# Performance work log

Measured on AMD Instinct MI355X. Metric: run time of the kernel, lower is better.

Reference implementation:

```python
import jax, jax.numpy as jnp
import numpy as np

CDECAY = 0.5      # NEURON_CDECAY = 1/2
VDECAY = 0.75     # NEURON_VDECAY = 3/4
VTH_INIT = 0.5
T = 50            # batch_window
sg = jax.lax.stop_gradient


@jax.custom_vjp
def pseudo_spike(v, vth):
    return (v > vth).astype(v.dtype)

def _ps_fwd(v, vth):
    return pseudo_spike(v, vth), (v, vth)

def _ps_bwd(res, g):
    v, vth = res
    # PseudoSpikeRect: rectangular surrogate gradient, window 0.5; no grad to vth
    return (g * (jnp.abs(v - vth) < 0.5).astype(g.dtype), jnp.zeros_like(vth))

pseudo_spike.defvjp(_ps_fwd, _ps_bwd)


def lif_step(x_in, W, b, u, v_prev, s_prev, temporal):
    """One neuron_model_* call + the temporal-threshold update that follows it."""
    u = u * CDECAY + x_in @ W.T + b
    v = v_prev * VDECAY * (1.0 - s_prev) + u
    # energy threshold term uses detached volts in the original (numpy round-trip)
    energy = jnp.exp((sg(v_prev) - sg(v)) / 3.0) - 1.0
    vth = 0.5 * temporal + 0.5 * energy
    s = pseudo_spike(v, vth)
    vsg = sg(v)  # threshold chain never reaches the loss (custom fn has no vth grad)
    V_m = vsg.mean() - 0.2 * (vsg.max() - vsg.min())
    V_theta = vth.mean() - 0.2 * (vth.max() - vth.min())
    temporal_new = 0.01 * (vsg - V_m) + V_theta + jnp.log(1.0 + jnp.exp((vsg - V_m) / 4.0))
    return u, v, s, temporal_new


def _forward(x, fc1_u, fc1_v, fc1_s, fc2_u, fc2_v, fc2_s, fc3_u, fc3_v, fc3_s,
             fc4_u, fc4_v, fc4_s, W1, b1, W2, b2, W3, b3, W4, b4):
    B = x.shape[0]
    H = W1.shape[0]
    A = W4.shape[0]
    t1 = jnp.full((B, H), VTH_INIT, x.dtype)
    t2 = jnp.full((B, H), VTH_INIT, x.dtype)
    t3 = jnp.full((B, H), VTH_INIT, x.dtype)
    t4 = jnp.full((B, A), VTH_INIT, x.dtype)
    acc = jnp.zeros((B, A), x.dtype)
    xs = jnp.transpose(x, (2, 0, 1))  # [T, B, state_num]

    def step(carry, xt):
        (u1, v1, s1, tt1, u2, v2, s2, tt2, u3, v3, s3, tt3, u4, v4, s4, tt4, a) = carry
        u1, v1, s1, tt1 = lif_step(xt, W1, b1, u1, v1, s1, tt1)
        u2, v2, s2, tt2 = lif_step(s1, W2, b2, u2, v2, s2, tt2)
        u3, v3, s3, tt3 = lif_step(s2, W3, b3, u3, v3, s3, tt3)
        u4, v4, s4, tt4 = lif_step(s3, W4, b4, u4, v4, s4, tt4)
        a = a + s4
        return (u1, v1, s1, tt1, u2, v2, s2, tt2, u3, v3, s3, tt3, u4, v4, s4, tt4, a), None

    carry0 = (fc1_u, fc1_v, fc1_s, t1, fc2_u, fc2_v, fc2_s, t2,
              fc3_u, fc3_v, fc3_s, t3, fc4_u, fc4_v, fc4_s, t4, acc)
    carry, _ = jax.lax.scan(step, carry0, xs)
    return carry[-1] / T  # fc4_sumspike / batch_window


def setup_inputs() -> dict:
    key = jax.random.key(0)
    ks = jax.random.split(key, 10)
    B, S, H, A = 2048, 256, 256, 2
    inp = {"x": jax.random.normal(ks[0], (B, S, T), jnp.float32)}
    for name, shp in [("fc1_u", (B, H)), ("fc1_v", (B, H)), ("fc1_s", (B, H)),
                      ("fc2_u", (B, H)), ("fc2_v", (B, H)), ("fc2_s", (B, H)),
                      ("fc3_u", (B, H)), ("fc3_v", (B, H)), ("fc3_s", (B, H)),
                      ("fc4_u", (B, A)), ("fc4_v", (B, A)), ("fc4_s", (B, A))]:
        inp[name] = jnp.zeros(shp, jnp.float32)
    def lin(k, fan_out, fan_in):
        bound = 1.0 / np.sqrt(fan_in)
        kw, kb = jax.random.split(k)
        W = jax.random.uniform(kw, (fan_out, fan_in), jnp.float32, -bound, bound)
        b = jax.random.uniform(kb, (fan_out,), jnp.float32, -bound, bound)
        return W, b
    inp["W1"], inp["b1"] = lin(ks[1], H, S)
    inp["W2"], inp["b2"] = lin(ks[2], H, H)
    inp["W3"], inp["b3"] = lin(ks[3], H, H)
    inp["W4"], inp["b4"] = lin(ks[4], A, H)
    inp["batch_size"] = B
    return inp


def reference(x, fc1_u, fc1_v, fc1_s, fc2_u, fc2_v, fc2_s, fc3_u, fc3_v, fc3_s,
              fc4_u, fc4_v, fc4_s, W1, b1, W2, b2, W3, b3, W4, b4, batch_size):
    return _forward(x, fc1_u, fc1_v, fc1_s, fc2_u, fc2_v, fc2_s,
                    fc3_u, fc3_v, fc3_s, fc4_u, fc4_v, fc4_s,
                    W1, b1, W2, b2, W3, b3, W4, b4)
```

## Files before the change

kernel.cpp:

```cpp
#include <hip/hip_runtime.h>
#include <cstdint>
#include <cstddef>

#define BB 2048
#define SS 256
#define HH 256
#define AA 2
#define TT 50
#define ROWS  32
#define NTHR  512
#define NLG   64
#define NGRID 192
#define KSTR  272
#define WLAYER (256 * KSTR)
#define LSTR  36
#define S3P   260

struct Params {
  const float* x;
  const float* fu[3]; const float* fv[3]; const float* fs[3];
  const float* f4u; const float* f4v; const float* f4s;
  const float* W[3]; const float* bs[3];
  const float* W4; const float* b4;
  float* out;
  float* wt3;
  float* partials;
  unsigned* flags;
  float* sbuf;
  float* xT;
  int use_xt;
};

__device__ __forceinline__ void pstore(float* p, float v) {
  __hip_atomic_store(p, v, __ATOMIC_RELAXED, __HIP_MEMORY_SCOPE_AGENT);
}
__device__ __forceinline__ float pload(const float* p) {
  return __hip_atomic_load(p, __ATOMIC_RELAXED, __HIP_MEMORY_SCOPE_AGENT);
}
__device__ __forceinline__ unsigned uload_acq(const unsigned* p) {
  return __hip_atomic_load(p, __ATOMIC_ACQUIRE, __HIP_MEMORY_SCOPE_AGENT);
}
__device__ __forceinline__ void ustore_rel(unsigned* p, unsigned v) {
  __hip_atomic_store(p, v, __ATOMIC_RELEASE, __HIP_MEMORY_SCOPE_AGENT);
}
__device__ __forceinline__ void uadd(unsigned* p) {
  __hip_atomic_fetch_add(p, 1u, __ATOMIC_ACQ_REL, __HIP_MEMORY_SCOPE_AGENT);
}

#define OUTER(IV, WV)                                        \
  acc[0][0] = fmaf((IV).x, (WV).x, acc[0][0]);               \
  acc[0][1] = fmaf((IV).x, (WV).y, acc[0][1]);               \
  acc[0][2] = fmaf((IV).x, (WV).z, acc[0][2]);               \
  acc[0][3] = fmaf((IV).x, (WV).w, acc[0][3]);               \
  acc[1][0] = fmaf((IV).y, (WV).x, acc[1][0]);               \
  acc[1][1] = fmaf((IV).y, (WV).y, acc[1][1]);               \
  acc[1][2] = fmaf((IV).y, (WV).z, acc[1][2]);               \
  acc[1][3] = fmaf((IV).y, (WV).w, acc[1][3]);               \
  acc[2][0] = fmaf((IV).z, (WV).x, acc[2][0]);               \
  acc[2][1] = fmaf((IV).z, (WV).y, acc[2][1]);               \
  acc[2][2] = fmaf((IV).z, (WV).z, acc[2][2]);               \
  acc[2][3] = fmaf((IV).z, (WV).w, acc[2][3]);               \
  acc[3][0] = fmaf((IV).w, (WV).x, acc[3][0]);               \
  acc[3][1] = fmaf((IV).w, (WV).y, acc[3][1]);               \
  acc[3][2] = fmaf((IV).w, (WV).z, acc[3][2]);               \
  acc[3][3] = fmaf((IV).w, (WV).w, acc[3][3]);

__global__ __launch_bounds__(NTHR, 2)
void snn_pipe(Params p) {
#pragma clang fp contract(off)
  const int tid = threadIdx.x;
  const int blk = blockIdx.x;
  const int L   = blk >> 6;
  const int g   = blk & 63;
  const int B0  = g * ROWS;

  const int w    = tid >> 6;
  const int l    = tid & 63;
  const int hp   = w & 3;
  const int qp   = w >> 2;
  const int hsel = l & 15;
  const int jsel = l >> 4;
  const int hb   = hp * 64 + hsel * 4;
  const int jb   = qp * 16 + jsel * 4;

  const int sid = tid & 255;
  const int jq  = tid >> 8;

  __shared__ __align__(16) float in_lds[HH * LSTR];
  __shared__ __align__(16) float s3_lds[ROWS * S3P];
  __shared__ float wred[8][6];
  __shared__ float scal[2][2];
  __shared__ float l4u[64], l4v[64], l4s[64], l4t[64],
                   l4acc[64], l4vn[64], l4vth[64];

  {
    const int gtid = blk * NTHR + tid;
    if (gtid < 16384) {
      const int h = gtid & 255, kq = gtid >> 8;
      #pragma unroll
      for (int ll = 0; ll < 3; ++ll) {
        float4 wv = *reinterpret_cast<const float4*>(p.W[ll] + (size_t)h * 256 + kq * 4);
        float* dst = p.wt3 + (size_t)ll * WLAYER + (size_t)(kq * 4) * KSTR + h;
        dst[0 * KSTR] = wv.x; dst[1 * KSTR] = wv.y;
        dst[2 * KSTR] = wv.z; dst[3 * KSTR] = wv.w;
      }
    }
    if (p.use_xt) {
      for (int sid0 = gtid; sid0 < BB * SS; sid0 += NGRID * NTHR) {
        const float* src = p.x + (size_t)sid0 * TT;
        #pragma unroll 1
        for (int t = 0; t < TT; ++t)
          p.xT[(size_t)t * (BB * SS) + sid0] = src[t];
      }
    }
  }

  float u[4][4], v[4][4], tp[4][4];
  unsigned smask = 0;
  #pragma unroll
  for (int jj = 0; jj < 4; ++jj) {
    size_t idx = (size_t)(B0 + jb + jj) * HH + hb;
    float4 uu = *reinterpret_cast<const float4*>(p.fu[L] + idx);
    float4 vv = *reinterpret_cast<const float4*>(p.fv[L] + idx);
    float4 ss = *reinterpret_cast<const float4*>(p.fs[L] + idx);
    u[jj][0] = uu.x; u[jj][1] = uu.y; u[jj][2] = uu.z; u[jj][3] = uu.w;
    v[jj][0] = vv.x; v[jj][1] = vv.y; v[jj][2] = vv.z; v[jj][3] = vv.w;
    if (ss.x != 0.0f) smask |= 1u << (jj * 4 + 0);
    if (ss.y != 0.0f) smask |= 1u << (jj * 4 + 1);
    if (ss.z != 0.0f) smask |= 1u << (jj * 4 + 2);
    if (ss.w != 0.0f) smask |= 1u << (jj * 4 + 3);
    #pragma unroll
    for (int i = 0; i < 4; ++i) tp[jj][i] = 0.5f;
  }
  const float4 bb4 = *reinterpret_cast<const float4*>(p.bs[L] + hb);
  const float bL[4] = { bb4.x, bb4.y, bb4.z, bb4.w };
  if (L == 2 && tid < 64) {
    size_t idx = (size_t)(B0 + (tid >> 1)) * AA + (tid & 1);
    l4u[tid] = p.f4u[idx]; l4v[tid] = p.f4v[idx]; l4s[tid] = p.f4s[idx];
    l4t[tid] = 0.5f; l4acc[tid] = 0.0f;
  }
  __syncthreads();

  if (tid == 0) {
    uadd(&p.flags[260]);
    while (uload_acq(&p.flags[260]) < (unsigned)NGRID) __builtin_amdgcn_s_sleep(2);
  }
  __syncthreads();

  const float* wbase = p.wt3 + (size_t)L * WLAYER + hb;
  float* sb_in  = (L > 0) ? p.sbuf + (size_t)(L - 1) * 2 * BB * HH : nullptr;
  float* sb_out = (L < 2) ? p.sbuf + (size_t)L * 2 * BB * HH : nullptr;

  #pragma unroll 1
  for (int t = 0; t < TT; ++t) {
    if (L == 0) {
      if (p.use_xt) {
        const float* base = p.xT + (size_t)t * (BB * SS) + (size_t)B0 * SS;
        #pragma unroll
        for (int iq = 0; iq < 4; ++iq) {
          const int j = jq * 16 + iq * 4;
          float4 vv = make_float4(base[(size_t)(j + 0) * SS + sid],
                                  base[(size_t)(j + 1) * SS + sid],
                                  base[(size_t)(j + 2) * SS + sid],
                                  base[(size_t)(j + 3) * SS + sid]);
          *reinterpret_cast<float4*>(&in_lds[sid * LSTR + j]) = vv;
        }
      } else {
        #pragma unroll
        for (int iq = 0; iq < 4; ++iq) {
          const int j = jq * 16 + iq * 4;
          float4 vv = make_float4(
              p.x[((size_t)(B0 + j + 0) * SS + sid) * TT + t],
              p.x[((size_t)(B0 + j + 1) * SS + sid) * TT + t],
              p.x[((size_t)(B0 + j + 2) * SS + sid) * TT + t],
              p.x[((size_t)(B0 + j + 3) * SS + sid) * TT + t]);
          *reinterpret_cast<float4*>(&in_lds[sid * LSTR + j]) = vv;
        }
      }
    } else {
      const int hop = L - 1;
      if (tid == 0) {
        while (uload_acq(&p.flags[hop * 64 + g]) < (unsigned)(t + 1))
          __builtin_amdgcn_s_sleep(2);
      }
      __syncthreads();
      const float* src = sb_in + (size_t)(t & 1) * BB * HH;
      #pragma unroll
      for (int iq = 0; iq < 4; ++iq) {
        const int j = jq * 16 + iq * 4;
        float4 vv = make_float4(pload(src + (size_t)(B0 + j + 0) * HH + sid),
                                pload(src + (size_t)(B0 + j + 1) * HH + sid),
                                pload(src + (size_t)(B0 + j + 2) * HH + sid),
                                pload(src + (size_t)(B0 + j + 3) * HH + sid));
        *reinterpret_cast<float4*>(&in_lds[sid * LSTR + j]) = vv;
      }
      __syncthreads();
      if (tid == 0) ustore_rel(&p.flags[128 + hop * 64 + g], (unsigned)(t + 1));
    }
    __syncthreads();

    float acc[4][4];
    #pragma unroll
    for (int jj = 0; jj < 4; ++jj)
      #pragma unroll
      for (int i = 0; i < 4; ++i) acc[jj][i] = 0.0f;
    #pragma unroll 2
    for (int k4 = 0; k4 < 64; ++k4) {
      const float* wk = wbase + (size_t)(k4 * 4) * KSTR;
      float4 w0 = *reinterpret_cast<const float4*>(wk);
      float4 w1 = *reinterpret_cast<const float4*>(wk + KSTR);
      float4 w2 = *reinterpret_cast<const float4*>(wk + 2 * KSTR);
      float4 w3 = *reinterpret_cast<const float4*>(wk + 3 * KSTR);
      const float* ib = &in_lds[(k4 * 4) * LSTR + jb];
      float4 i0 = *reinterpret_cast<const float4*>(ib);
      float4 i1 = *reinterpret_cast<const float4*>(ib + LSTR);
      float4 i2 = *reinterpret_cast<const float4*>(ib + 2 * LSTR);
      float4 i3 = *reinterpret_cast<const float4*>(ib + 3 * LSTR);
      OUTER(i0, w0);
      OUTER(i1, w1);
      OUTER(i2, w2);
      OUTER(i3, w3);
    }

    if (t > 0) {
      if (tid == 0) {
        while (uload_acq(&p.flags[256 + L]) < (unsigned)(NLG * t))
          __builtin_amdgcn_s_sleep(2);
      }
      __syncthreads();
      {
        const int wv = tid >> 6, ln = tid & 63;
        if (wv == 0 || (wv == 1 && L == 2)) {
          const int ch = (wv == 0) ? L : 3;
          const float* pb = p.partials + (size_t)(ch * 2 + ((t - 1) & 1)) * 6 * 64;
          float r[6];
          #pragma unroll
          for (int st = 0; st < 6; ++st) {
            float rr = pload(pb + st * 64 + ln);
            if (st == 0 || st == 3) {
              #pragma unroll
              for (int m = 1; m < 64; m <<= 1) rr += __shfl_xor(rr, m);
            } else if (st == 1 || st == 4) {
              #pragma unroll
              for (int m = 1; m < 64; m <<= 1) rr = fmaxf(rr, __shfl_xor(rr, m));
            } else {
              #pragma unroll
              for (int m = 1; m < 64; m <<= 1) rr = fminf(rr, __shfl_xor(rr, m));
            }
            r[st] = rr;
          }
          if (ln == 0) {
            const float invN = (ch == 3) ? (1.0f / 4096.0f) : (1.0f / 524288.0f);
            scal[wv][0] = (r[0] * invN) - 0.2f * (r[1] - r[2]);
            scal[wv][1] = (r[3] * invN) - 0.2f * (r[4] - r[5]);
          }
        }
      }
      __syncthreads();
      {
        const float Vm = scal[0][0], Vt = scal[0][1];
        #pragma unroll
        for (int jj = 0; jj < 4; ++jj)
          #pragma unroll
          for (int i = 0; i < 4; ++i) {
            float d = v[jj][i] - Vm;
            float sp = logf(1.0f + expf(d * 0.25f));
            tp[jj][i] = (0.01f * d + Vt) + sp;
          }
      }
      if (L == 2 && tid < 64) {
        const float Vm = scal[1][0], Vt = scal[1][1];
        float d = l4v[tid] - Vm;
        float sp = logf(1.0f + expf(d * 0.25f));
        l4t[tid] = (0.01f * d + Vt) + sp;
      }
      __syncthreads();
    }

    float sv = 0.f, svt = 0.f;
    float mxv = -3.402823466e38f, mnv = 3.402823466e38f;
    float mxvt = -3.402823466e38f, mnvt = 3.402823466e38f;
    unsigned nsmask = 0;
    #pragma unroll
    for (int jj = 0; jj < 4; ++jj) {
      #pragma unroll
      for (int i = 0; i < 4; ++i) {
        float un = fmaf(u[jj][i], 0.5f, acc[jj][i]) + bL[i];
        float vp = v[jj][i];
        float vd = ((smask >> (jj * 4 + i)) & 1u) ? 0.0f : vp * 0.75f;
        float vn = vd + un;
        float en = expf((vp - vn) / 3.0f) - 1.0f;
        float vt = 0.5f * tp[jj][i] + 0.5f * en;
        const bool sx = vn > vt;
        u[jj][i] = un; v[jj][i] = vn;
        if (sx) nsmask |= 1u << (jj * 4 + i);
        sv += vn; svt += vt;
        mxv = fmaxf(mxv, vn); mnv = fminf(mnv, vn);
        mxvt = fmaxf(mxvt, vt); mnvt = fminf(mnvt, vt);
      }
    }
    smask = nsmask;
    #pragma unroll
    for (int m = 1; m < 64; m <<= 1) {
      sv += __shfl_xor(sv, m);   svt += __shfl_xor(svt, m);
      mxv = fmaxf(mxv, __shfl_xor(mxv, m));  mnv = fminf(mnv, __shfl_xor(mnv, m));
      mxvt = fmaxf(mxvt, __shfl_xor(mxvt, m)); mnvt = fminf(mnvt, __shfl_xor(mnvt, m));
    }
    if ((tid & 63) == 0) {
      int wv = tid >> 6;
      wred[wv][0] = sv;  wred[wv][1] = mxv;  wred[wv][2] = mnv;
      wred[wv][3] = svt; wred[wv][4] = mxvt; wred[wv][5] = mnvt;
    }
    #pragma unroll
    for (int jj = 0; jj < 4; ++jj) {
      *reinterpret_cast<float4*>(&s3_lds[(jb + jj) * S3P + hb]) = make_float4(
          ((nsmask >> (jj * 4 + 0)) & 1u) ? 1.0f : 0.0f,
          ((nsmask >> (jj * 4 + 1)) & 1u) ? 1.0f : 0.0f,
          ((nsmask >> (jj * 4 + 2)) & 1u) ? 1.0f : 0.0f,
          ((nsmask >> (jj * 4 + 3)) & 1u) ? 1.0f : 0.0f);
    }
    __syncthreads();

    if (L < 2) {
      if (tid < 6) {
        const int st = tid;
        float r = wred[0][st];
        if (st == 0 || st == 3) {
          #pragma unroll
          for (int wv = 1; wv < 8; ++wv) r = r + wred[wv][st];
        } else if (st == 1 || st == 4) {
          #pragma unroll
          for (int wv = 1; wv < 8; ++wv) r = fmaxf(r, wred[wv][st]);
        } else {
          #pragma unroll
          for (int wv = 1; wv < 8; ++wv) r = fminf(r, wred[wv][st]);
        }
        pstore(p.partials + (size_t)(L * 2 + (t & 1)) * 6 * 64 + st * 64 + g, r);
      }
      if (t >= 2 && tid == 1) {
        while (uload_acq(&p.flags[128 + L * 64 + g]) < (unsigned)(t - 1))
          __builtin_amdgcn_s_sleep(2);
      }
      __syncthreads();
      if (tid == 0) uadd(&p.flags[256 + L]);
      float* dst = sb_out + (size_t)(t & 1) * BB * HH;
      #pragma unroll
      for (int jr = 0; jr < 16; ++jr) {
        const int j = jq * 16 + jr;
        pstore(dst + (size_t)(B0 + j) * HH + sid, s3_lds[j * S3P + sid]);
      }
      __syncthreads();
      if (tid == 0) ustore_rel(&p.flags[L * 64 + g], (unsigned)(t + 1));
    } else {
      if (tid < 6) {
        const int st = tid;
        float r = wred[0][st];
        if (st == 0 || st == 3) {
          #pragma unroll
          for (int wv = 1; wv < 8; ++wv) r = r + wred[wv][st];
        } else if (st == 1 || st == 4) {
          #pragma unroll
          for (int wv = 1; wv < 8; ++wv) r = fmaxf(r, wred[wv][st]);
        } else {
          #pragma unroll
          for (int wv = 1; wv < 8; ++wv) r = fminf(r, wred[wv][st]);
        }
        pstore(p.partials + (size_t)(2 * 2 + (t & 1)) * 6 * 64 + st * 64 + g, r);
      }
      __syncthreads();

      {
        const int d = tid >> 3, c = tid & 7;
        if (d < 64) {
          const int j4 = d >> 1, a4 = d & 1;
          float part = 0.0f;
          #pragma unroll
          for (int i = 0; i < 32; ++i) {
            int k = c + 8 * i;
            part = fmaf(s3_lds[j4 * S3P + k], p.W4[a4 * HH + k], part);
          }
          #pragma unroll
          for (int m = 1; m < 8; m <<= 1) part += __shfl_xor(part, m);
          if (c == 0) {
            float un = fmaf(l4u[d], 0.5f, part) + p.b4[a4];
            float vp = l4v[d];
            float vd = (vp * 0.75f) * (1.0f - l4s[d]);
            float vn = vd + un;
            float en = expf((vp - vn) / 3.0f) - 1.0f;
            float vt = 0.5f * l4t[d] + 0.5f * en;
            float sx = (vn > vt) ? 1.0f : 0.0f;
            l4u[d] = un; l4v[d] = vn; l4s[d] = sx;
            l4acc[d] += sx; l4vn[d] = vn; l4vth[d] = vt;
          }
        }
      }
      __syncthreads();

      if (tid < 64) {
        float a = l4vn[tid], b = l4vth[tid];
        float s4 = a, mx4 = a, mn4 = a;
        float st4 = b, mxt4 = b, mnt4 = b;
        #pragma unroll
        for (int m = 1; m < 64; m <<= 1) {
          s4  += __shfl_xor(s4, m);   st4 += __shfl_xor(st4, m);
          mx4  = fmaxf(mx4,  __shfl_xor(mx4, m));  mn4  = fminf(mn4,  __shfl_xor(mn4, m));
          mxt4 = fmaxf(mxt4, __shfl_xor(mxt4, m)); mnt4 = fminf(mnt4, __shfl_xor(mnt4, m));
        }
        if (tid == 0) {
          float* pp = p.partials + (size_t)(3 * 2 + (t & 1)) * 6 * 64 + g;
          pstore(pp + 0 * 64, s4);   pstore(pp + 1 * 64, mx4);  pstore(pp + 2 * 64, mn4);
          pstore(pp + 3 * 64, st4);  pstore(pp + 4 * 64, mxt4); pstore(pp + 5 * 64, mnt4);
        }
      }
      __syncthreads();
      if (tid == 0) uadd(&p.flags[256 + L]);
    }
  }

  if (L == 2 && tid < 64)
    p.out[(size_t)(B0 + (tid >> 1)) * AA + (tid & 1)] = l4acc[tid] / 50.0f;
}

extern "C" void kernel_launch(void* const* d_in, const int* in_sizes, int n_in,
                              void* d_out, int out_size, void* d_ws, size_t ws_size,
                              hipStream_t stream) {
  Params p;
  p.x     = (const float*)d_in[0];
  p.fu[0] = (const float*)d_in[1];  p.fv[0] = (const float*)d_in[2];  p.fs[0] = (const float*)d_in[3];
  p.fu[1] = (const float*)d_in[4];  p.fv[1] = (const float*)d_in[5];  p.fs[1] = (const float*)d_in[6];
  p.fu[2] = (const float*)d_in[7];  p.fv[2] = (const float*)d_in[8];  p.fs[2] = (const float*)d_in[9];
  p.f4u   = (const float*)d_in[10]; p.f4v   = (const float*)d_in[11]; p.f4s   = (const float*)d_in[12];
  p.W[0]  = (const float*)d_in[13]; p.bs[0] = (const float*)d_in[14];
  p.W[1]  = (const float*)d_in[15]; p.bs[1] = (const float*)d_in[16];
  p.W[2]  = (const float*)d_in[17]; p.bs[2] = (const float*)d_in[18];
  p.W4    = (const float*)d_in[19]; p.b4    = (const float*)d_in[20];
  p.out   = (float*)d_out;

  float* ws   = (float*)d_ws;
  p.wt3       = ws;
  p.partials  = ws + 208896;
  p.flags     = (unsigned*)(ws + 211968);
  p.sbuf      = ws + 212992;
  p.xT        = ws + 2310144;
  size_t need = ((size_t)2310144 + (size_t)TT * BB * SS) * sizeof(float);
  p.use_xt    = (ws_size >= need) ? 1 : 0;

  hipMemsetAsync((void*)p.flags, 0, 4096, stream);
  snn_pipe<<<dim3(NGRID), dim3(NTHR), 0, stream>>>(p);
}
```

Measured before the change: 1.890 ms.

## Split layer 4 into its own pipeline stage and pass spikes as bytes

Adds a fourth group of 64 blocks, raising the grid from 192 to 256, so the small output layer (fc4) runs as its own pipeline stage instead of being serialized behind layer 3 inside the same blocks. Inter-stage spike buffers switch from float to uint8, cutting the handoff traffic through global memory by a factor of four, and the flag and workspace layout are re-indexed to match. The extra stage adds another hop of synchronisation latency and needs all 256 blocks to be co-resident for the spin-wait barriers to avoid deadlock.

```diff
diff --git a/kernel.cpp b/kernel.cpp
--- a/kernel.cpp
+++ b/kernel.cpp
@@ -10,7 +10,7 @@
 #define ROWS  32
 #define NTHR  512
 #define NLG   64
-#define NGRID 192
+#define NGRID 256
 #define KSTR  272
 #define WLAYER (256 * KSTR)
 #define LSTR  36
@@ -26,7 +26,7 @@
   float* wt3;
   float* partials;
   unsigned* flags;
-  float* sbuf;
+  uint8_t* sbuf;
   float* xT;
   int use_xt;
 };
@@ -35,6 +35,12 @@
   __hip_atomic_store(p, v, __ATOMIC_RELAXED, __HIP_MEMORY_SCOPE_AGENT);
 }
 __device__ __forceinline__ float pload(const float* p) {
+  return __hip_atomic_load(p, __ATOMIC_RELAXED, __HIP_MEMORY_SCOPE_AGENT);
+}
+__device__ __forceinline__ void bstore(uint8_t* p, uint8_t v) {
+  __hip_atomic_store(p, v, __ATOMIC_RELAXED, __HIP_MEMORY_SCOPE_AGENT);
+}
+__device__ __forceinline__ uint8_t bload(const uint8_t* p) {
   return __hip_atomic_load(p, __ATOMIC_RELAXED, __HIP_MEMORY_SCOPE_AGENT);
 }
 __device__ __forceinline__ unsigned uload_acq(const unsigned* p) {
@@ -73,6 +79,7 @@
   const int L   = blk >> 6;
   const int g   = blk & 63;
   const int B0  = g * ROWS;
+  const int LW  = (L < 3) ? L : 2;
 
   const int w    = tid >> 6;
   const int l    = tid & 63;
@@ -89,7 +96,7 @@
   __shared__ __align__(16) float in_lds[HH * LSTR];
   __shared__ __align__(16) float s3_lds[ROWS * S3P];
   __shared__ float wred[8][6];
-  __shared__ float scal[2][2];
+  __shared__ float scal[2];
   __shared__ float l4u[64], l4v[64], l4s[64], l4t[64],
                    l4acc[64], l4vn[64], l4vth[64];
 
@@ -116,25 +123,27 @@
   }
 
   float u[4][4], v[4][4], tp[4][4];
+  float bL[4] = {0.f, 0.f, 0.f, 0.f};
   unsigned smask = 0;
-  #pragma unroll
-  for (int jj = 0; jj < 4; ++jj) {
-    size_t idx = (size_t)(B0 + jb + jj) * HH + hb;
-    float4 uu = *reinterpret_cast<const float4*>(p.fu[L] + idx);
-    float4 vv = *reinterpret_cast<const float4*>(p.fv[L] + idx);
-    float4 ss = *reinterpret_cast<const float4*>(p.fs[L] + idx);
-    u[jj][0] = uu.x; u[jj][1] = uu.y; u[jj][2] = uu.z; u[jj][3] = uu.w;
-    v[jj][0] = vv.x; v[jj][1] = vv.y; v[jj][2] = vv.z; v[jj][3] = vv.w;
-    if (ss.x != 0.0f) smask |= 1u << (jj * 4 + 0);
-    if (ss.y != 0.0f) smask |= 1u << (jj * 4 + 1);
-    if (ss.z != 0.0f) smask |= 1u << (jj * 4 + 2);
-    if (ss.w != 0.0f) smask |= 1u << (jj * 4 + 3);
+  if (L < 3) {
     #pragma unroll
-    for (int i = 0; i < 4; ++i) tp[jj][i] = 0.5f;
-  }
-  const float4 bb4 = *reinterpret_cast<const float4*>(p.bs[L] + hb);
-  const float bL[4] = { bb4.x, bb4.y, bb4.z, bb4.w };
-  if (L == 2 && tid < 64) {
+    for (int jj = 0; jj < 4; ++jj) {
+      size_t idx = (size_t)(B0 + jb + jj) * HH + hb;
+      float4 uu = *reinterpret_cast<const float4*>(p.fu[LW] + idx);
+      float4 vv = *reinterpret_cast<const float4*>(p.fv[LW] + idx);
+      float4 ss = *reinterpret_cast<const float4*>(p.fs[LW] + idx);
+      u[jj][0] = uu.x; u[jj][1] = uu.y; u[jj][2] = uu.z; u[jj][3] = uu.w;
+      v[jj][0] = vv.x; v[jj][1] = vv.y; v[jj][2] = vv.z; v[jj][3] = vv.w;
+      if (ss.x != 0.0f) smask |= 1u << (jj * 4 + 0);
+      if (ss.y != 0.0f) smask |= 1u << (jj * 4 + 1);
+      if (ss.z != 0.0f) smask |= 1u << (jj * 4 + 2);
+      if (ss.w != 0.0f) smask |= 1u << (jj * 4 + 3);
+      #pragma unroll
+      for (int i = 0; i < 4; ++i) tp[jj][i] = 0.5f;
+    }
+    float4 bb4 = *reinterpret_cast<const float4*>(p.bs[LW] + hb);
+    bL[0] = bb4.x; bL[1] = bb4.y; bL[2] = bb4.z; bL[3] = bb4.w;
+  } else if (tid < 64) {
     size_t idx = (size_t)(B0 + (tid >> 1)) * AA + (tid & 1);
     l4u[tid] = p.f4u[idx]; l4v[tid] = p.f4v[idx]; l4s[tid] = p.f4s[idx];
     l4t[tid] = 0.5f; l4acc[tid] = 0.0f;
@@ -142,101 +151,102 @@
   __syncthreads();
 
   if (tid == 0) {
-    uadd(&p.flags[260]);
-    while (uload_acq(&p.flags[260]) < (unsigned)NGRID) __builtin_amdgcn_s_sleep(2);
+    uadd(&p.flags[520]);
+    while (uload_acq(&p.flags[520]) < (unsigned)NGRID) __builtin_amdgcn_s_sleep(2);
   }
   __syncthreads();
 
-  const float* wbase = p.wt3 + (size_t)L * WLAYER + hb;
-  float* sb_in  = (L > 0) ? p.sbuf + (size_t)(L - 1) * 2 * BB * HH : nullptr;
-  float* sb_out = (L < 2) ? p.sbuf + (size_t)L * 2 * BB * HH : nullptr;
+  const float* wbase = p.wt3 + (size_t)LW * WLAYER + hb;
+  const uint8_t* sb_in = (L > 0) ? p.sbuf + (size_t)(L - 1) * 2 * BB * HH : nullptr;
+  uint8_t* sb_out      = (L < 3) ? p.sbuf + (size_t)L * 2 * BB * HH : nullptr;
 
   #pragma unroll 1
   for (int t = 0; t < TT; ++t) {
-    if (L == 0) {
-      if (p.use_xt) {
-        const float* base = p.xT + (size_t)t * (BB * SS) + (size_t)B0 * SS;
-        #pragma unroll
-        for (int iq = 0; iq < 4; ++iq) {
-          const int j = jq * 16 + iq * 4;
-          float4 vv = make_float4(base[(size_t)(j + 0) * SS + sid],
-                                  base[(size_t)(j + 1) * SS + sid],
-                                  base[(size_t)(j + 2) * SS + sid],
-                                  base[(size_t)(j + 3) * SS + sid]);
-          *reinterpret_cast<float4*>(&in_lds[sid * LSTR + j]) = vv;
+    const int par = t & 1;
+
+    if (L < 3) {
+      if (L == 0) {
+        if (p.use_xt) {
+          const float* base = p.xT + (size_t)t * (BB * SS) + (size_t)B0 * SS;
+          #pragma unroll
+          for (int iq = 0; iq < 4; ++iq) {
+            const int j = jq * 16 + iq * 4;
+            float4 vv = make_float4(base[(size_t)(j + 0) * SS + sid],
+                                    base[(size_t)(j + 1) * SS + sid],
+                                    base[(size_t)(j + 2) * SS + sid],
+                                    base[(size_t)(j + 3) * SS + sid]);
+            *reinterpret_cast<float4*>(&in_lds[sid * LSTR + j]) = vv;
+          }
+        } else {
+          #pragma unroll
+          for (int iq = 0; iq < 4; ++iq) {
+            const int j = jq * 16 + iq * 4;
+            float4 vv = make_float4(
+                p.x[((size_t)(B0 + j + 0) * SS + sid) * TT + t],
+                p.x[((size_t)(B0 + j + 1) * SS + sid) * TT + t],
+                p.x[((size_t)(B0 + j + 2) * SS + sid) * TT + t],
+                p.x[((size_t)(B0 + j + 3) * SS + sid) * TT + t]);
+            *reinterpret_cast<float4*>(&in_lds[sid * LSTR + j]) = vv;
+          }
         }
       } else {
+        const int hop = L - 1;
+        if (tid == 0) {
+          while (uload_acq(&p.flags[hop * 64 + g]) < (unsigned)(t + 1))
+            __builtin_amdgcn_s_sleep(2);
+        }
+        __syncthreads();
+        const uint8_t* src = sb_in + (size_t)par * BB * HH;
         #pragma unroll
         for (int iq = 0; iq < 4; ++iq) {
           const int j = jq * 16 + iq * 4;
           float4 vv = make_float4(
-              p.x[((size_t)(B0 + j + 0) * SS + sid) * TT + t],
-              p.x[((size_t)(B0 + j + 1) * SS + sid) * TT + t],
-              p.x[((size_t)(B0 + j + 2) * SS + sid) * TT + t],
-              p.x[((size_t)(B0 + j + 3) * SS + sid) * TT + t]);
+              (float)bload(src + (size_t)(B0 + j + 0) * HH + sid),
+              (float)bload(src + (size_t)(B0 + j + 1) * HH + sid),
+              (float)bload(src + (size_t)(B0 + j + 2) * HH + sid),
+              (float)bload(src + (size_t)(B0 + j + 3) * HH + sid));
           *reinterpret_cast<float4*>(&in_lds[sid * LSTR + j]) = vv;
         }
-      }
-    } else {
-      const int hop = L - 1;
-      if (tid == 0) {
-        while (uload_acq(&p.flags[hop * 64 + g]) < (unsigned)(t + 1))
-          __builtin_amdgcn_s_sleep(2);
-      }
-      __syncthreads();
-      const float* src = sb_in + (size_t)(t & 1) * BB * HH;
-      #pragma unroll
-      for (int iq = 0; iq < 4; ++iq) {
-        const int j = jq * 16 + iq * 4;
-        float4 vv = make_float4(pload(src + (size_t)(B0 + j + 0) * HH + sid),
-                                pload(src + (size_t)(B0 + j + 1) * HH + sid),
-                                pload(src + (size_t)(B0 + j + 2) * HH + sid),
-                                pload(src + (size_t)(B0 + j + 3) * HH + sid));
-        *reinterpret_cast<float4*>(&in_lds[sid * LSTR + j]) = vv;
-      }
-      __syncthreads();
-      if (tid == 0) ustore_rel(&p.flags[128 + hop * 64 + g], (unsigned)(t + 1));
-    }
-    __syncthreads();
-
-    float acc[4][4];
-    #pragma unroll
-    for (int jj = 0; jj < 4; ++jj)
-      #pragma unroll
-      for (int i = 0; i < 4; ++i) acc[jj][i] = 0.0f;
-    #pragma unroll 2
-    for (int k4 = 0; k4 < 64; ++k4) {
-      const float* wk = wbase + (size_t)(k4 * 4) * KSTR;
-      float4 w0 = *reinterpret_cast<const float4*>(wk);
-      float4 w1 = *reinterpret_cast<const float4*>(wk + KSTR);
-      float4 w2 = *reinterpret_cast<const float4*>(wk + 2 * KSTR);
-      float4 w3 = *reinterpret_cast<const float4*>(wk + 3 * KSTR);
-      const float* ib = &in_lds[(k4 * 4) * LSTR + jb];
-      float4 i0 = *reinterpret_cast<const float4*>(ib);
-      float4 i1 = *reinterpret_cast<const float4*>(ib + LSTR);
-      float4 i2 = *reinterpret_cast<const float4*>(ib + 2 * LSTR);
-      float4 i3 = *reinterpret_cast<const float4*>(ib + 3 * LSTR);
-      OUTER(i0, w0);
-      OUTER(i1, w1);
-      OUTER(i2, w2);
-      OUTER(i3, w3);
-    }
-
-    if (t > 0) {
-      if (tid == 0) {
-        while (uload_acq(&p.flags[256 + L]) < (unsigned)(NLG * t))
-          __builtin_amdgcn_s_sleep(2);
-      }
-      __syncthreads();
-      {
-        const int wv = tid >> 6, ln = tid & 63;
-        if (wv == 0 || (wv == 1 && L == 2)) {
-          const int ch = (wv == 0) ? L : 3;
-          const float* pb = p.partials + (size_t)(ch * 2 + ((t - 1) & 1)) * 6 * 64;
+        __syncthreads();
+        if (tid == 0) ustore_rel(&p.flags[256 + hop * 64 + g], (unsigned)(t + 1));
+      }
+      __syncthreads();
+
+      float acc[4][4];
+      #pragma unroll
+      for (int jj = 0; jj < 4; ++jj)
+        #pragma unroll
+        for (int i = 0; i < 4; ++i) acc[jj][i] = 0.0f;
+      #pragma unroll 2
+      for (int k4 = 0; k4 < 64; ++k4) {
+        const float* wk = wbase + (size_t)(k4 * 4) * KSTR;
+        float4 w0 = *reinterpret_cast<const float4*>(wk);
+        float4 w1 = *reinterpret_cast<const float4*>(wk + KSTR);
+        float4 w2 = *reinterpret_cast<const float4*>(wk + 2 * KSTR);
+        float4 w3 = *reinterpret_cast<const float4*>(wk + 3 * KSTR);
+        const float* ib = &in_lds[(k4 * 4) * LSTR + jb];
+        float4 i0 = *reinterpret_cast<const float4*>(ib);
+        float4 i1 = *reinterpret_cast<const float4*>(ib + LSTR);
+        float4 i2 = *reinterpret_cast<const float4*>(ib + 2 * LSTR);
+        float4 i3 = *reinterpret_cast<const float4*>(ib + 3 * LSTR);
+        OUTER(i0, w0);
+        OUTER(i1, w1);
+        OUTER(i2, w2);
+        OUTER(i3, w3);
+      }
+
+      if (t > 0) {
+        if (tid == 0) {
+          while (uload_acq(&p.flags[512 + L]) < (unsigned)(NLG * t))
+            __builtin_amdgcn_s_sleep(2);
+        }
+        __syncthreads();
+        if (w == 0) {
+          const float* pb = p.partials + (size_t)(L * 2 + ((t - 1) & 1)) * 6 * 64;
           float r[6];
           #pragma unroll
           for (int st = 0; st < 6; ++st) {
-            float rr = pload(pb + st * 64 + ln);
+            float rr = pload(pb + st * 64 + l);
             if (st == 0 || st == 3) {
               #pragma unroll
               for (int m = 1; m < 64; m <<= 1) rr += __shfl_xor(rr, m);
@@ -249,16 +259,14 @@
             }
             r[st] = rr;
           }
-          if (ln == 0) {
-            const float invN = (ch == 3) ? (1.0f / 4096.0f) : (1.0f / 524288.0f);
-            scal[wv][0] = (r[0] * invN) - 0.2f * (r[1] - r[2]);
-            scal[wv][1] = (r[3] * invN) - 0.2f * (r[4] - r[5]);
-          }
-        }
-      }
-      __syncthreads();
-      {
-        const float Vm = scal[0][0], Vt = scal[0][1];
+          if (l == 0) {
+            const float invN = 1.0f / 524288.0f;
+            scal[0] = (r[0] * invN) - 0.2f * (r[1] - r[2]);
+            scal[1] = (r[3] * invN) - 0.2f * (r[4] - r[5]);
+          }
+        }
+        __syncthreads();
+        const float Vm = scal[0], Vt = scal[1];
         #pragma unroll
         for (int jj = 0; jj < 4; ++jj)
           #pragma unroll
@@ -267,61 +275,53 @@
             float sp = logf(1.0f + expf(d * 0.25f));
             tp[jj][i] = (0.01f * d + Vt) + sp;
           }
-      }
-      if (L == 2 && tid < 64) {
-        const float Vm = scal[1][0], Vt = scal[1][1];
-        float d = l4v[tid] - Vm;
-        float sp = logf(1.0f + expf(d * 0.25f));
-        l4t[tid] = (0.01f * d + Vt) + sp;
-      }
-      __syncthreads();
-    }
-
-    float sv = 0.f, svt = 0.f;
-    float mxv = -3.402823466e38f, mnv = 3.402823466e38f;
-    float mxvt = -3.402823466e38f, mnvt = 3.402823466e38f;
-    unsigned nsmask = 0;
-    #pragma unroll
-    for (int jj = 0; jj < 4; ++jj) {
-      #pragma unroll
-      for (int i = 0; i < 4; ++i) {
-        float un = fmaf(u[jj][i], 0.5f, acc[jj][i]) + bL[i];
-        float vp = v[jj][i];
-        float vd = ((smask >> (jj * 4 + i)) & 1u) ? 0.0f : vp * 0.75f;
-        float vn = vd + un;
-        float en = expf((vp - vn) / 3.0f) - 1.0f;
-        float vt = 0.5f * tp[jj][i] + 0.5f * en;
-        const bool sx = vn > vt;
-        u[jj][i] = un; v[jj][i] = vn;
-        if (sx) nsmask |= 1u << (jj * 4 + i);
-        sv += vn; svt += vt;
-        mxv = fmaxf(mxv, vn); mnv = fminf(mnv, vn);
-        mxvt = fmaxf(mxvt, vt); mnvt = fminf(mnvt, vt);
-      }
-    }
-    smask = nsmask;
-    #pragma unroll
-    for (int m = 1; m < 64; m <<= 1) {
-      sv += __shfl_xor(sv, m);   svt += __shfl_xor(svt, m);
-      mxv = fmaxf(mxv, __shfl_xor(mxv, m));  mnv = fminf(mnv, __shfl_xor(mnv, m));
-      mxvt = fmaxf(mxvt, __shfl_xor(mxvt, m)); mnvt = fminf(mnvt, __shfl_xor(mnvt, m));
-    }
-    if ((tid & 63) == 0) {
-      int wv = tid >> 6;
-      wred[wv][0] = sv;  wred[wv][1] = mxv;  wred[wv][2] = mnv;
-      wred[wv][3] = svt; wred[wv][4] = mxvt; wred[wv][5] = mnvt;
-    }
-    #pragma unroll
-    for (int jj = 0; jj < 4; ++jj) {
-      *reinterpret_cast<float4*>(&s3_lds[(jb + jj) * S3P + hb]) = make_float4(
-          ((nsmask >> (jj * 4 + 0)) & 1u) ? 1.0f : 0.0f,
-          ((nsmask >> (jj * 4 + 1)) & 1u) ? 1.0f : 0.0f,
-          ((nsmask >> (jj * 4 + 2)) & 1u) ? 1.0f : 0.0f,
-          ((nsmask >> (jj * 4 + 3)) & 1u) ? 1.0f : 0.0f);
-    }
-    __syncthreads();
-
-    if (L < 2) {
+        __syncthreads();
+      }
+
+      float sv = 0.f, svt = 0.f;
+      float mxv = -3.402823466e38f, mnv = 3.402823466e38f;
+      float mxvt = -3.402823466e38f, mnvt = 3.402823466e38f;
+      unsigned nsmask = 0;
+      #pragma unroll
+      for (int jj = 0; jj < 4; ++jj) {
+        #pragma unroll
+        for (int i = 0; i < 4; ++i) {
+          float un = fmaf(u[jj][i], 0.5f, acc[jj][i]) + bL[i];
+          float vp = v[jj][i];
+          float vd = ((smask >> (jj * 4 + i)) & 1u) ? 0.0f : vp * 0.75f;
+          float vn = vd + un;
+          float en = expf((vp - vn) / 3.0f) - 1.0f;
+          float vt = 0.5f * tp[jj][i] + 0.5f * en;
+          const bool sx = vn > vt;
+          u[jj][i] = un; v[jj][i] = vn;
+          if (sx) nsmask |= 1u << (jj * 4 + i);
+          sv += vn; svt += vt;
+          mxv = fmaxf(mxv, vn); mnv = fminf(mnv, vn);
+          mxvt = fmaxf(mxvt, vt); mnvt = fminf(mnvt, vt);
+        }
+      }
+      smask = nsmask;
+      #pragma unroll
+      for (int m = 1; m < 64; m <<= 1) {
+        sv += __shfl_xor(sv, m);   svt += __shfl_xor(svt, m);
+        mxv = fmaxf(mxv, __shfl_xor(mxv, m));  mnv = fminf(mnv, __shfl_xor(mnv, m));
+        mxvt = fmaxf(mxvt, __shfl_xor(mxvt, m)); mnvt = fminf(mnvt, __shfl_xor(mnvt, m));
+      }
+      if ((tid & 63) == 0) {
+        int wv = tid >> 6;
+        wred[wv][0] = sv;  wred[wv][1] = mxv;  wred[wv][2] = mnv;
+        wred[wv][3] = svt; wred[wv][4] = mxvt; wred[wv][5] = mnvt;
+      }
+      #pragma unroll
+      for (int jj = 0; jj < 4; ++jj) {
+        *reinterpret_cast<float4*>(&s3_lds[(jb + jj) * S3P + hb]) = make_float4(
+            ((nsmask >> (jj * 4 + 0)) & 1u) ? 1.0f : 0.0f,
+            ((nsmask >> (jj * 4 + 1)) & 1u) ? 1.0f : 0.0f,
+            ((nsmask >> (jj * 4 + 2)) & 1u) ? 1.0f : 0.0f,
+            ((nsmask >> (jj * 4 + 3)) & 1u) ? 1.0f : 0.0f);
+      }
+      __syncthreads();
+
       if (tid < 6) {
         const int st = tid;
         float r = wred[0][st];
@@ -335,63 +335,101 @@
           #pragma unroll
           for (int wv = 1; wv < 8; ++wv) r = fminf(r, wred[wv][st]);
         }
-        pstore(p.partials + (size_t)(L * 2 + (t & 1)) * 6 * 64 + st * 64 + g, r);
+        pstore(p.partials + (size_t)(L * 2 + par) * 6 * 64 + st * 64 + g, r);
       }
       if (t >= 2 && tid == 1) {
-        while (uload_acq(&p.flags[128 + L * 64 + g]) < (unsigned)(t - 1))
+        while (uload_acq(&p.flags[256 + L * 64 + g]) < (unsigned)(t - 1))
           __builtin_amdgcn_s_sleep(2);
       }
       __syncthreads();
-      if (tid == 0) uadd(&p.flags[256 + L]);
-      float* dst = sb_out + (size_t)(t & 1) * BB * HH;
+      if (tid == 0) uadd(&p.flags[512 + L]);
+      uint8_t* dst = sb_out + (size_t)par * BB * HH;
       #pragma unroll
       for (int jr = 0; jr < 16; ++jr) {
         const int j = jq * 16 + jr;
-        pstore(dst + (size_t)(B0 + j) * HH + sid, s3_lds[j * S3P + sid]);
+        bstore(dst + (size_t)(B0 + j) * HH + sid,
+               (uint8_t)(s3_lds[j * S3P + sid] != 0.0f ? 1 : 0));
       }
       __syncthreads();
       if (tid == 0) ustore_rel(&p.flags[L * 64 + g], (unsigned)(t + 1));
     } else {
-      if (tid < 6) {
-        const int st = tid;
-        float r = wred[0][st];
-        if (st == 0 || st == 3) {
-          #pragma unroll
-          for (int wv = 1; wv < 8; ++wv) r = r + wred[wv][st];
-        } else if (st == 1 || st == 4) {
-          #pragma unroll
-          for (int wv = 1; wv < 8; ++wv) r = fmaxf(r, wred[wv][st]);
-        } else {
-          #pragma unroll
-          for (int wv = 1; wv < 8; ++wv) r = fminf(r, wred[wv][st]);
-        }
-        pstore(p.partials + (size_t)(2 * 2 + (t & 1)) * 6 * 64 + st * 64 + g, r);
-      }
-      __syncthreads();
+      if (tid == 0) {
+        while (uload_acq(&p.flags[2 * 64 + g]) < (unsigned)(t + 1))
+          __builtin_amdgcn_s_sleep(2);
+      }
+      __syncthreads();
+      {
+        const uint8_t* src = sb_in + (size_t)par * BB * HH;
+        #pragma unroll
+        for (int jr = 0; jr < 16; ++jr) {
+          const int j = jq * 16 + jr;
+          s3_lds[j * S3P + sid] = (float)bload(src + (size_t)(B0 + j) * HH + sid);
+        }
+      }
+      __syncthreads();
+      if (tid == 0) ustore_rel(&p.flags[256 + 2 * 64 + g], (unsigned)(t + 1));
+
+      if (t > 0) {
+        if (tid == 0) {
+          while (uload_acq(&p.flags[512 + 3]) < (unsigned)(NLG * t))
+            __builtin_amdgcn_s_sleep(2);
+        }
+        __syncthreads();
+        if (w == 0) {
+          const float* pb = p.partials + (size_t)(3 * 2 + ((t - 1) & 1)) * 6 * 64;
+          float r[6];
+          #pragma unroll
+          for (int st = 0; st < 6; ++st) {
+            float rr = pload(pb + st * 64 + l);
+            if (st == 0 || st == 3) {
+              #pragma unroll
+              for (int m = 1; m < 64; m <<= 1) rr += __shfl_xor(rr, m);
+            } else if (st == 1 || st == 4) {
+              #pragma unroll
+              for (int m = 1; m < 64; m <<= 1) rr = fmaxf(rr, __shfl_xor(rr, m));
+            } else {
+              #pragma unroll
+              for (int m = 1; m < 64; m <<= 1) rr = fminf(rr, __shfl_xor(rr, m));
+            }
+            r[st] = rr;
+          }
+          if (l == 0) {
+            const float invN = 1.0f / 4096.0f;
+            scal[0] = (r[0] * invN) - 0.2f * (r[1] - r[2]);
+            scal[1] = (r[3] * invN) - 0.2f * (r[4] - r[5]);
+          }
+        }
+        __syncthreads();
+        if (tid < 64) {
+          const float Vm = scal[0], Vt = scal[1];
+          float d = l4v[tid] - Vm;
+          float sp = logf(1.0f + expf(d * 0.25f));
+          l4t[tid] = (0.01f * d + Vt) + sp;
+        }
+        __syncthreads();
+      }
 
       {
         const int d = tid >> 3, c = tid & 7;
-        if (d < 64) {
-          const int j4 = d >> 1, a4 = d & 1;
-          float part = 0.0f;
-          #pragma unroll
-          for (int i = 0; i < 32; ++i) {
-            int k = c + 8 * i;
-            part = fmaf(s3_lds[j4 * S3P + k], p.W4[a4 * HH + k], part);
-          }
-          #pragma unroll
-          for (int m = 1; m < 8; m <<= 1) part += __shfl_xor(part, m);
-          if (c == 0) {
-            float un = fmaf(l4u[d], 0.5f, part) + p.b4[a4];
-            float vp = l4v[d];
-            float vd = (vp * 0.75f) * (1.0f - l4s[d]);
-            float vn = vd + un;
-            float en = expf((vp - vn) / 3.0f) - 1.0f;
-            float vt = 0.5f * l4t[d] + 0.5f * en;
-            float sx = (vn > vt) ? 1.0f : 0.0f;
-            l4u[d] = un; l4v[d] = vn; l4s[d] = sx;
-            l4acc[d] += sx; l4vn[d] = vn; l4vth[d] = vt;
-          }
+        const int j4 = d >> 1, a4 = d & 1;
+        float part = 0.0f;
+        #pragma unroll
+        for (int i = 0; i < 32; ++i) {
+          int k = c + 8 * i;
+          part = fmaf(s3_lds[j4 * S3P + k], p.W4[a4 * HH + k], part);
+        }
+        #pragma unroll
+        for (int m = 1; m < 8; m <<= 1) part += __shfl_xor(part, m);
+        if (c == 0) {
+          float un = fmaf(l4u[d], 0.5f, part) + p.b4[a4];
+          float vp = l4v[d];
+          float vd = (vp * 0.75f) * (1.0f - l4s[d]);
+          float vn = vd + un;
+          float en = expf((vp - vn) / 3.0f) - 1.0f;
+          float vt = 0.5f * l4t[d] + 0.5f * en;
+          float sx = (vn > vt) ? 1.0f : 0.0f;
+          l4u[d] = un; l4v[d] = vn; l4s[d] = sx;
+          l4acc[d] += sx; l4vn[d] = vn; l4vth[d] = vt;
         }
       }
       __syncthreads();
@@ -407,17 +445,17 @@
           mxt4 = fmaxf(mxt4, __shfl_xor(mxt4, m)); mnt4 = fminf(mnt4, __shfl_xor(mnt4, m));
         }
         if (tid == 0) {
-          float* pp = p.partials + (size_t)(3 * 2 + (t & 1)) * 6 * 64 + g;
+          float* pp = p.partials + (size_t)(3 * 2 + par) * 6 * 64 + g;
           pstore(pp + 0 * 64, s4);   pstore(pp + 1 * 64, mx4);  pstore(pp + 2 * 64, mn4);
           pstore(pp + 3 * 64, st4);  pstore(pp + 4 * 64, mxt4); pstore(pp + 5 * 64, mnt4);
         }
       }
       __syncthreads();
-      if (tid == 0) uadd(&p.flags[256 + L]);
+      if (tid == 0) uadd(&p.flags[512 + 3]);
     }
   }
 
-  if (L == 2 && tid < 64)
+  if (L == 3 && tid < 64)
     p.out[(size_t)(B0 + (tid >> 1)) * AA + (tid & 1)] = l4acc[tid] / 50.0f;
 }
 
@@ -440,9 +478,9 @@
   p.wt3       = ws;
   p.partials  = ws + 208896;
   p.flags     = (unsigned*)(ws + 211968);
-  p.sbuf      = ws + 212992;
-  p.xT        = ws + 2310144;
-  size_t need = ((size_t)2310144 + (size_t)TT * BB * SS) * sizeof(float);
+  p.sbuf      = (uint8_t*)(ws + 212992);
+  p.xT        = ws + 409600;
+  size_t need = ((size_t)409600 + (size_t)TT * BB * SS) * sizeof(float);
   p.use_xt    = (ws_size >= need) ? 1 : 0;
 
   hipMemsetAsync((void*)p.flags, 0, 4096, stream);
```

New measurement: 2.150 ms. 13.7% more time.
